# Kernel tuning notes

Measured on AMD Instinct MI355X. Metric: run time of the kernel, lower is better.

The kernel has to match this reference:

```python
import jax, jax.numpy as jnp
import numpy as np

EPS = 1e-12
B, CNT = 4096, 2048

def setup_inputs() -> dict:
    key = jax.random.key(0)
    k1, k2, k3 = jax.random.split(key, 3)
    timestampns_set = jax.random.uniform(k1, (B, CNT), dtype=jnp.float32)
    gyro_set = jax.random.normal(k2, (B, CNT, 3), dtype=jnp.float32)
    start_quat = jax.random.normal(k3, (B, 4), dtype=jnp.float32)
    # conv1/conv2 reduce to 3x3 linear maps on the xyz axis; initialized to identity, bias 0
    W1 = jnp.eye(3, dtype=jnp.float32)
    b1 = jnp.zeros((3,), dtype=jnp.float32)
    a1 = jnp.float32(0.25)  # PReLU default, single shared parameter
    W2 = jnp.eye(3, dtype=jnp.float32)
    b2 = jnp.zeros((3,), dtype=jnp.float32)
    a2 = jnp.float32(0.25)
    return {"timestampns_set": timestampns_set, "gyro_set": gyro_set,
            "start_quat": start_quat, "W1": W1, "b1": b1, "a1": a1,
            "W2": W2, "b2": b2, "a2": a2}

def _prelu(x, a):
    return jnp.where(x >= 0, x, a * x)

def _qmul(a, b):
    aw, ax, ay, az = a[:, 0], a[:, 1], a[:, 2], a[:, 3]
    bw, bx, by, bz = b[:, 0], b[:, 1], b[:, 2], b[:, 3]
    ow = aw * bw - ax * bx - ay * by - az * bz
    ox = aw * bx + ax * bw + ay * bz - az * by
    oy = aw * by - ax * bz + ay * bw + az * bx
    oz = aw * bz + ax * by - ay * bx + az * bw
    return jnp.stack((ow, ox, oy, oz), axis=-1)

def reference(timestampns_set, gyro_set, start_quat, W1, b1, a1, W2, b2, a2):
    # calibrate_gyro: two identity-init 3x3 'convs' + PReLU, residual add
    h = _prelu(jnp.einsum('btc,oc->bto', gyro_set, W1) + b1, a1)
    g = _prelu(jnp.einsum('btc,oc->bto', h, W2) + b2, a2) + gyro_set  # [B,CNT,3]
    dt = timestampns_set[:, 1:] - timestampns_set[:, :-1]             # [B,CNT-1]
    gm = 0.5 * (g[:, :-1, :] + g[:, 1:, :])                            # midpoint gyro
    dtheta_half = gm * dt[:, :, None] * 0.5                           # [B,CNT-1,3]

    def step(q, d):
        dq = jnp.concatenate([jnp.ones((d.shape[0], 1), d.dtype), d], axis=1)
        q = _qmul(q, dq)
        n = jnp.sqrt(jnp.sum(q * q, axis=1, keepdims=True))
        q = q / jnp.maximum(n, EPS)  # F.normalize semantics
        return q, None

    q, _ = jax.lax.scan(step, start_quat, jnp.swapaxes(dtheta_half, 0, 1))
    return q
```

## Files before the change

### kernel.cpp

```cpp
#include <hip/hip_runtime.h>

#define CNT   2048
#define NSTEP 2047
#define TPB   256
#define CHUNK 8
#define NWAVE (TPB / 64)

struct Q { float w, x, y, z; };

__device__ inline Q qmul(const Q a, const Q b) {
    Q o;
    o.w = a.w*b.w - a.x*b.x - a.y*b.y - a.z*b.z;
    o.x = a.w*b.x + a.x*b.w + a.y*b.z - a.z*b.y;
    o.y = a.w*b.y - a.x*b.z + a.y*b.w + a.z*b.x;
    o.z = a.w*b.z + a.x*b.y - a.y*b.x + a.z*b.w;
    return o;
}

__device__ inline Q qmul1(const Q a, const float bx, const float by, const float bz) {
    Q o;
    o.w = a.w - (a.x*bx + a.y*by + a.z*bz);
    o.x = a.x + (a.w*bx + a.y*bz - a.z*by);
    o.y = a.y + (a.w*by - a.x*bz + a.z*bx);
    o.z = a.z + (a.w*bz + a.x*by - a.y*bx);
    return o;
}

__global__ __launch_bounds__(TPB) void quat_scan_kernel(
    const float* __restrict__ ts,
    const float* __restrict__ gyro,
    const float* __restrict__ sq,
    const float* __restrict__ W1, const float* __restrict__ b1, const float* __restrict__ a1p,
    const float* __restrict__ W2, const float* __restrict__ b2, const float* __restrict__ a2p,
    float* __restrict__ out)
{
    __shared__ Q s_q[NWAVE];

    const int b    = blockIdx.x;
    const int tid  = threadIdx.x;
    const int t0   = tid * CHUNK;
    const bool last = (tid == TPB - 1);

    float rg[28];
    {
        const float4* gp = (const float4*)(gyro + (size_t)b * (CNT * 3) + (size_t)t0 * 3);
        #pragma unroll
        for (int k = 0; k < 6; ++k) ((float4*)rg)[k] = gp[k];
        if (!last) {
            ((float4*)rg)[6] = gp[6];
        } else {
            ((float4*)rg)[6] = make_float4(0.f, 0.f, 0.f, 0.f);
        }
    }
    float rt[9];
    {
        const float4* tp = (const float4*)(ts + (size_t)b * CNT + t0);
        #pragma unroll
        for (int k = 0; k < 2; ++k) ((float4*)&rt[0])[k] = tp[k];
        rt[8] = last ? rt[7] : ts[(size_t)b * CNT + t0 + 8];
    }

    float w1[9], w2[9], bb1[3], bb2[3];
    #pragma unroll
    for (int i = 0; i < 9; ++i) { w1[i] = W1[i]; w2[i] = W2[i]; }
    #pragma unroll
    for (int i = 0; i < 3; ++i) { bb1[i] = b1[i]; bb2[i] = b2[i]; }
    const float a1 = a1p[0], a2 = a2p[0];

    auto gf = [&](int j, float& gx, float& gy, float& gz) {
        const float vx = rg[3*j + 0], vy = rg[3*j + 1], vz = rg[3*j + 2];
        float h0 = w1[0]*vx + w1[1]*vy + w1[2]*vz + bb1[0];
        float h1 = w1[3]*vx + w1[4]*vy + w1[5]*vz + bb1[1];
        float h2 = w1[6]*vx + w1[7]*vy + w1[8]*vz + bb1[2];
        h0 = h0 >= 0.0f ? h0 : a1 * h0;
        h1 = h1 >= 0.0f ? h1 : a1 * h1;
        h2 = h2 >= 0.0f ? h2 : a1 * h2;
        float u0 = w2[0]*h0 + w2[1]*h1 + w2[2]*h2 + bb2[0];
        float u1 = w2[3]*h0 + w2[4]*h1 + w2[5]*h2 + bb2[1];
        float u2 = w2[6]*h0 + w2[7]*h1 + w2[8]*h2 + bb2[2];
        u0 = u0 >= 0.0f ? u0 : a2 * u0;
        u1 = u1 >= 0.0f ? u1 : a2 * u1;
        u2 = u2 >= 0.0f ? u2 : a2 * u2;
        gx = u0 + vx; gy = u1 + vy; gz = u2 + vz;
    };

    Q q = {1.0f, 0.0f, 0.0f, 0.0f};
    float g0x, g0y, g0z;
    gf(0, g0x, g0y, g0z);
    #pragma unroll
    for (int j = 0; j < CHUNK; ++j) {
        float g1x, g1y, g1z;
        gf(j + 1, g1x, g1y, g1z);
        const float s = 0.25f * (rt[j + 1] - rt[j]);
        q = qmul1(q, (g0x + g1x) * s, (g0y + g1y) * s, (g0z + g1z) * s);
        g0x = g1x; g0y = g1y; g0z = g1z;
    }

    {
        const float n2  = q.w*q.w + q.x*q.x + q.y*q.y + q.z*q.z;
        const float inv = 1.0f / sqrtf(n2);
        q.w *= inv; q.x *= inv; q.y *= inv; q.z *= inv;
    }

    #pragma unroll
    for (int sft = 1; sft < 64; sft <<= 1) {
        Q o;
        o.w = __shfl_down(q.w, sft);
        o.x = __shfl_down(q.x, sft);
        o.y = __shfl_down(q.y, sft);
        o.z = __shfl_down(q.z, sft);
        q = qmul(q, o);
    }

    const int lane = tid & 63;
    const int wid  = tid >> 6;
    if (lane == 0) s_q[wid] = q;
    __syncthreads();

    if (tid == 0) {
        Q acc = s_q[0];
        #pragma unroll
        for (int w = 1; w < NWAVE; ++w) acc = qmul(acc, s_q[w]);

        const float4 s0 = ((const float4*)(sq + (size_t)b * 4))[0];
        const Q q0 = {s0.x, s0.y, s0.z, s0.w};
        Q qf = qmul(q0, acc);
        const float n   = sqrtf(qf.w*qf.w + qf.x*qf.x + qf.y*qf.y + qf.z*qf.z);
        const float inv = 1.0f / fmaxf(n, 1e-12f);
        float4 o;
        o.x = qf.w * inv; o.y = qf.x * inv; o.z = qf.y * inv; o.w = qf.z * inv;
        ((float4*)(out + (size_t)b * 4))[0] = o;
    }
}

extern "C" void kernel_launch(void* const* d_in, const int* in_sizes, int n_in,
                              void* d_out, int out_size, void* d_ws, size_t ws_size,
                              hipStream_t stream) {
    const float* ts   = (const float*)d_in[0];
    const float* gyro = (const float*)d_in[1];
    const float* sq   = (const float*)d_in[2];
    const float* W1   = (const float*)d_in[3];
    const float* b1   = (const float*)d_in[4];
    const float* a1   = (const float*)d_in[5];
    const float* W2   = (const float*)d_in[6];
    const float* b2   = (const float*)d_in[7];
    const float* a2   = (const float*)d_in[8];
    float* out = (float*)d_out;

    const int B = in_sizes[0] / CNT;

    quat_scan_kernel<<<B, TPB, 0, stream>>>(ts, gyro, sq, W1, b1, a1, W2, b2, a2, out);
}
```

Measured before the change: 185.9 us.

## Use one wave per row with double-buffered async global-to-LDS segment loads

Each batch row is now handled by a single 64-lane wave instead of a 256-thread block. The row is processed in 8 segments of 256 steps, streamed into LDS with global_load_lds and double-buffered so the next segment's loads overlap the current segment's compute. Each segment is reduced with a wave-level quaternion shuffle scan, and the segment products are accumulated in order. This removes the __syncthreads and shared-memory cross-wave combine, but it adds 8 shuffle reductions per row and relies on manually encoded waitcnt values.

```diff
diff --git a/kernel.cpp b/kernel.cpp
--- a/kernel.cpp
+++ b/kernel.cpp
@@ -1,14 +1,13 @@
 #include <hip/hip_runtime.h>
 
 #define CNT   2048
-#define NSTEP 2047
-#define TPB   256
-#define CHUNK 8
-#define NWAVE (TPB / 64)
+#define TPB   64
+#define NSEG  8
+#define SMEM_F 2560
 
 struct Q { float w, x, y, z; };
 
-__device__ inline Q qmul(const Q a, const Q b) {
+__device__ __forceinline__ Q qmul(const Q a, const Q b) {
     Q o;
     o.w = a.w*b.w - a.x*b.x - a.y*b.y - a.z*b.z;
     o.x = a.w*b.x + a.x*b.w + a.y*b.z - a.z*b.y;
@@ -16,14 +15,36 @@
     o.z = a.w*b.z + a.x*b.y - a.y*b.x + a.z*b.w;
     return o;
 }
-
-__device__ inline Q qmul1(const Q a, const float bx, const float by, const float bz) {
+__device__ __forceinline__ Q qmul1(const Q a, const float bx, const float by, const float bz) {
     Q o;
     o.w = a.w - (a.x*bx + a.y*by + a.z*bz);
     o.x = a.x + (a.w*bx + a.y*bz - a.z*by);
     o.y = a.y + (a.w*by - a.x*bz + a.z*bx);
     o.z = a.z + (a.w*bz + a.x*by - a.y*bx);
     return o;
+}
+
+typedef __attribute__((address_space(1))) const void GAS;
+typedef __attribute__((address_space(3))) void LAS;
+
+__device__ __forceinline__ void cp16(const void* g, void* l) {
+    __builtin_amdgcn_global_load_lds((GAS*)g, (LAS*)l, 16, 0, 0);
+}
+__device__ __forceinline__ void wait_vm5() { __builtin_amdgcn_s_waitcnt(0x0F75); }
+__device__ __forceinline__ void wait_vm4() { __builtin_amdgcn_s_waitcnt(0x0F74); }
+__device__ __forceinline__ void wait_vm0() { __builtin_amdgcn_s_waitcnt(0x0F70); }
+
+__device__ __forceinline__ void issue_seg(const char* grow, const char* trow,
+                                          float* smem, int s, int lane) {
+    char* gslot = (char*)(smem + ((s & 1) ? 1024 : 0));
+    char* tslot = (char*)(smem + 2048 + ((s & 1) ? 256 : 0));
+    const char* gs = grow + 3072 * s + 16 * lane;
+    const char* tsr = trow + 1024 * s + 16 * lane;
+    cp16(gs,        gslot);
+    cp16(gs + 1024, gslot + 1024);
+    cp16(gs + 2048, gslot + 2048);
+    if (s != 7) cp16(gs + 3072, gslot + 3072);
+    cp16(tsr, tslot);
 }
 
 __global__ __launch_bounds__(TPB) void quat_scan_kernel(
@@ -34,31 +55,13 @@
     const float* __restrict__ W2, const float* __restrict__ b2, const float* __restrict__ a2p,
     float* __restrict__ out)
 {
-    __shared__ Q s_q[NWAVE];
+    __shared__ float smem[SMEM_F];
 
     const int b    = blockIdx.x;
-    const int tid  = threadIdx.x;
-    const int t0   = tid * CHUNK;
-    const bool last = (tid == TPB - 1);
+    const int lane = threadIdx.x;
 
-    float rg[28];
-    {
-        const float4* gp = (const float4*)(gyro + (size_t)b * (CNT * 3) + (size_t)t0 * 3);
-        #pragma unroll
-        for (int k = 0; k < 6; ++k) ((float4*)rg)[k] = gp[k];
-        if (!last) {
-            ((float4*)rg)[6] = gp[6];
-        } else {
-            ((float4*)rg)[6] = make_float4(0.f, 0.f, 0.f, 0.f);
-        }
-    }
-    float rt[9];
-    {
-        const float4* tp = (const float4*)(ts + (size_t)b * CNT + t0);
-        #pragma unroll
-        for (int k = 0; k < 2; ++k) ((float4*)&rt[0])[k] = tp[k];
-        rt[8] = last ? rt[7] : ts[(size_t)b * CNT + t0 + 8];
-    }
+    const char* grow = (const char*)(gyro + (size_t)b * (CNT * 3));
+    const char* trow = (const char*)(ts   + (size_t)b * CNT);
 
     float w1[9], w2[9], bb1[3], bb2[3];
     #pragma unroll
@@ -67,8 +70,12 @@
     for (int i = 0; i < 3; ++i) { bb1[i] = b1[i]; bb2[i] = b2[i]; }
     const float a1 = a1p[0], a2 = a2p[0];
 
-    auto gf = [&](int j, float& gx, float& gy, float& gz) {
-        const float vx = rg[3*j + 0], vy = rg[3*j + 1], vz = rg[3*j + 2];
+    const float* trowf = (const float*)trow;
+    int bidx = 256 * (lane + 1); if (bidx > 2047) bidx = 2047;
+    const float tbound = trowf[bidx];
+
+    auto gf = [&](const float* rg, int k, float& gx, float& gy, float& gz) {
+        const float vx = rg[3*k + 0], vy = rg[3*k + 1], vz = rg[3*k + 2];
         float h0 = w1[0]*vx + w1[1]*vy + w1[2]*vz + bb1[0];
         float h1 = w1[3]*vx + w1[4]*vy + w1[5]*vz + bb1[1];
         float h2 = w1[6]*vx + w1[7]*vy + w1[8]*vz + bb1[2];
@@ -84,52 +91,76 @@
         gx = u0 + vx; gy = u1 + vy; gz = u2 + vz;
     };
 
-    Q q = {1.0f, 0.0f, 0.0f, 0.0f};
-    float g0x, g0y, g0z;
-    gf(0, g0x, g0y, g0z);
-    #pragma unroll
-    for (int j = 0; j < CHUNK; ++j) {
-        float g1x, g1y, g1z;
-        gf(j + 1, g1x, g1y, g1z);
-        const float s = 0.25f * (rt[j + 1] - rt[j]);
-        q = qmul1(q, (g0x + g1x) * s, (g0y + g1y) * s, (g0z + g1z) * s);
-        g0x = g1x; g0y = g1y; g0z = g1z;
+    Q qrow = {1.0f, 0.0f, 0.0f, 0.0f};
+
+    auto do_seg = [&](int s, bool fix_last) {
+        const float* gb = smem + ((s & 1) ? 1024 : 0);
+        const float* tb = smem + 2048 + ((s & 1) ? 256 : 0);
+
+        float rg[16];
+        const float4* gp4 = (const float4*)(gb + 12 * lane);
+        #pragma unroll
+        for (int k = 0; k < 4; ++k) ((float4*)rg)[k] = gp4[k];
+
+        float rt[5];
+        *((float4*)rt) = *((const float4*)(tb + 4 * lane));
+        float rt4 = tb[4 * lane + 4];
+        const float bnd = __shfl(tbound, s & 7);
+        rt[4] = (lane == 63) ? bnd : rt4;
+
+        if (fix_last && lane == 63) {
+            rg[12] = rg[9]; rg[13] = rg[10]; rg[14] = rg[11];
+            rt[4]  = rt[3];
+        }
+
+        Q P = {1.0f, 0.0f, 0.0f, 0.0f};
+        float g0x, g0y, g0z;
+        gf(rg, 0, g0x, g0y, g0z);
+        #pragma unroll
+        for (int j = 0; j < 4; ++j) {
+            float g1x, g1y, g1z;
+            gf(rg, j + 1, g1x, g1y, g1z);
+            const float sc = 0.25f * (rt[j + 1] - rt[j]);
+            P = qmul1(P, (g0x + g1x) * sc, (g0y + g1y) * sc, (g0z + g1z) * sc);
+            g0x = g1x; g0y = g1y; g0z = g1z;
+        }
+        const float n2  = P.w*P.w + P.x*P.x + P.y*P.y + P.z*P.z;
+        const float inv = 1.0f / sqrtf(n2);
+        P.w *= inv; P.x *= inv; P.y *= inv; P.z *= inv;
+
+        #pragma unroll
+        for (int sft = 1; sft < 64; sft <<= 1) {
+            Q o;
+            o.w = __shfl_down(P.w, sft);
+            o.x = __shfl_down(P.x, sft);
+            o.y = __shfl_down(P.y, sft);
+            o.z = __shfl_down(P.z, sft);
+            P = qmul(P, o);
+        }
+        qrow = qmul(qrow, P);
+    };
+
+    issue_seg(grow, trow, smem, 0, lane);
+    issue_seg(grow, trow, smem, 1, lane);
+    for (int s = 0; s < 6; ++s) {
+        wait_vm5();
+        do_seg(s, false);
+        issue_seg(grow, trow, smem, s + 2, lane);
     }
+    wait_vm4();
+    do_seg(6, false);
+    wait_vm0();
+    do_seg(7, true);
 
-    {
-        const float n2  = q.w*q.w + q.x*q.x + q.y*q.y + q.z*q.z;
-        const float inv = 1.0f / sqrtf(n2);
-        q.w *= inv; q.x *= inv; q.y *= inv; q.z *= inv;
-    }
-
-    #pragma unroll
-    for (int sft = 1; sft < 64; sft <<= 1) {
-        Q o;
-        o.w = __shfl_down(q.w, sft);
-        o.x = __shfl_down(q.x, sft);
-        o.y = __shfl_down(q.y, sft);
-        o.z = __shfl_down(q.z, sft);
-        q = qmul(q, o);
-    }
-
-    const int lane = tid & 63;
-    const int wid  = tid >> 6;
-    if (lane == 0) s_q[wid] = q;
-    __syncthreads();
-
-    if (tid == 0) {
-        Q acc = s_q[0];
-        #pragma unroll
-        for (int w = 1; w < NWAVE; ++w) acc = qmul(acc, s_q[w]);
-
-        const float4 s0 = ((const float4*)(sq + (size_t)b * 4))[0];
+    if (lane == 0) {
+        const float4 s0 = *((const float4*)(sq + (size_t)b * 4));
         const Q q0 = {s0.x, s0.y, s0.z, s0.w};
-        Q qf = qmul(q0, acc);
+        Q qf = qmul(q0, qrow);
         const float n   = sqrtf(qf.w*qf.w + qf.x*qf.x + qf.y*qf.y + qf.z*qf.z);
         const float inv = 1.0f / fmaxf(n, 1e-12f);
         float4 o;
         o.x = qf.w * inv; o.y = qf.x * inv; o.z = qf.y * inv; o.w = qf.z * inv;
-        ((float4*)(out + (size_t)b * 4))[0] = o;
+        *((float4*)(out + (size_t)b * 4)) = o;
     }
 }
 
```

After: 194.9 us. 1.05x slower.

## Split scan into persistent wave-per-segment pass plus combine pass, with identity fast path

Applied to the files above, without the earlier changes.

Restructures the kernel so each wavefront handles one quarter-row segment in a grid-stride persistent loop, with software prefetching of the next segment's inputs into registers. Per-segment quaternion products go to workspace, and a second small kernel multiplies the four segments and applies the start quaternion. This removes the block-level shared memory and barrier and is meant to improve latency hiding. It also adds a runtime check that skips the 3x3 matmuls when the weights are exactly identity with zero bias. The cost is an extra kernel launch and higher register pressure from the double buffers.

```diff
diff --git a/kernel.cpp b/kernel.cpp
--- a/kernel.cpp
+++ b/kernel.cpp
@@ -1,14 +1,14 @@
 #include <hip/hip_runtime.h>
 
-#define CNT   2048
-#define NSTEP 2047
-#define TPB   256
-#define CHUNK 8
-#define NWAVE (TPB / 64)
+#define CNT    2048
+#define NSTEP  2047
+#define TPB    256
+#define BLOCKS 2048
+#define WPB    (TPB / 64)
 
 struct Q { float w, x, y, z; };
 
-__device__ inline Q qmul(const Q a, const Q b) {
+__device__ __forceinline__ Q qmul(const Q a, const Q b) {
     Q o;
     o.w = a.w*b.w - a.x*b.x - a.y*b.y - a.z*b.z;
     o.x = a.w*b.x + a.x*b.w + a.y*b.z - a.z*b.y;
@@ -16,8 +16,7 @@
     o.z = a.w*b.z + a.x*b.y - a.y*b.x + a.z*b.w;
     return o;
 }
-
-__device__ inline Q qmul1(const Q a, const float bx, const float by, const float bz) {
+__device__ __forceinline__ Q qmul1(const Q a, const float bx, const float by, const float bz) {
     Q o;
     o.w = a.w - (a.x*bx + a.y*by + a.z*bz);
     o.x = a.x + (a.w*bx + a.y*bz - a.z*by);
@@ -26,39 +25,78 @@
     return o;
 }
 
-__global__ __launch_bounds__(TPB) void quat_scan_kernel(
+template<bool FAST>
+__device__ __forceinline__ void gf_eval(const float* rg, int k,
+        const float* w1, const float* bb1, float a1,
+        const float* w2, const float* bb2, float a2,
+        float& gx, float& gy, float& gz)
+{
+    const float vx = rg[3*k + 0], vy = rg[3*k + 1], vz = rg[3*k + 2];
+    float h0, h1, h2;
+    if (FAST) { h0 = vx; h1 = vy; h2 = vz; }
+    else {
+        h0 = w1[0]*vx + w1[1]*vy + w1[2]*vz + bb1[0];
+        h1 = w1[3]*vx + w1[4]*vy + w1[5]*vz + bb1[1];
+        h2 = w1[6]*vx + w1[7]*vy + w1[8]*vz + bb1[2];
+    }
+    h0 = h0 >= 0.0f ? h0 : a1 * h0;
+    h1 = h1 >= 0.0f ? h1 : a1 * h1;
+    h2 = h2 >= 0.0f ? h2 : a1 * h2;
+    float u0, u1, u2;
+    if (FAST) { u0 = h0; u1 = h1; u2 = h2; }
+    else {
+        u0 = w2[0]*h0 + w2[1]*h1 + w2[2]*h2 + bb2[0];
+        u1 = w2[3]*h0 + w2[4]*h1 + w2[5]*h2 + bb2[1];
+        u2 = w2[6]*h0 + w2[7]*h1 + w2[8]*h2 + bb2[2];
+    }
+    u0 = u0 >= 0.0f ? u0 : a2 * u0;
+    u1 = u1 >= 0.0f ? u1 : a2 * u1;
+    u2 = u2 >= 0.0f ? u2 : a2 * u2;
+    gx = u0 + vx; gy = u1 + vy; gz = u2 + vz;
+}
+
+template<bool FAST>
+__device__ __forceinline__ Q seg_product(const float* rg, const float* rt,
+        const float* w1, const float* bb1, float a1,
+        const float* w2, const float* bb2, float a2)
+{
+    Q P = {1.0f, 0.0f, 0.0f, 0.0f};
+    float g0x, g0y, g0z;
+    gf_eval<FAST>(rg, 0, w1, bb1, a1, w2, bb2, a2, g0x, g0y, g0z);
+    #pragma unroll
+    for (int j = 0; j < 8; ++j) {
+        float g1x, g1y, g1z;
+        gf_eval<FAST>(rg, j + 1, w1, bb1, a1, w2, bb2, a2, g1x, g1y, g1z);
+        const float sc = 0.25f * (rt[j + 1] - rt[j]);
+        P = qmul1(P, (g0x + g1x) * sc, (g0y + g1y) * sc, (g0z + g1z) * sc);
+        g0x = g1x; g0y = g1y; g0z = g1z;
+    }
+    const float n2  = P.w*P.w + P.x*P.x + P.y*P.y + P.z*P.z;
+    const float inv = 1.0f / sqrtf(n2);
+    P.w *= inv; P.x *= inv; P.y *= inv; P.z *= inv;
+    #pragma unroll
+    for (int sft = 1; sft < 64; sft <<= 1) {
+        Q o;
+        o.w = __shfl_down(P.w, sft);
+        o.x = __shfl_down(P.x, sft);
+        o.y = __shfl_down(P.y, sft);
+        o.z = __shfl_down(P.z, sft);
+        P = qmul(P, o);
+    }
+    return P;
+}
+
+__global__ __launch_bounds__(TPB) void pass1_kernel(
     const float* __restrict__ ts,
     const float* __restrict__ gyro,
-    const float* __restrict__ sq,
     const float* __restrict__ W1, const float* __restrict__ b1, const float* __restrict__ a1p,
     const float* __restrict__ W2, const float* __restrict__ b2, const float* __restrict__ a2p,
-    float* __restrict__ out)
+    float4* __restrict__ ws,
+    int nitems)
 {
-    __shared__ Q s_q[NWAVE];
-
-    const int b    = blockIdx.x;
-    const int tid  = threadIdx.x;
-    const int t0   = tid * CHUNK;
-    const bool last = (tid == TPB - 1);
-
-    float rg[28];
-    {
-        const float4* gp = (const float4*)(gyro + (size_t)b * (CNT * 3) + (size_t)t0 * 3);
-        #pragma unroll
-        for (int k = 0; k < 6; ++k) ((float4*)rg)[k] = gp[k];
-        if (!last) {
-            ((float4*)rg)[6] = gp[6];
-        } else {
-            ((float4*)rg)[6] = make_float4(0.f, 0.f, 0.f, 0.f);
-        }
-    }
-    float rt[9];
-    {
-        const float4* tp = (const float4*)(ts + (size_t)b * CNT + t0);
-        #pragma unroll
-        for (int k = 0; k < 2; ++k) ((float4*)&rt[0])[k] = tp[k];
-        rt[8] = last ? rt[7] : ts[(size_t)b * CNT + t0 + 8];
-    }
+    const int lane = threadIdx.x & 63;
+    const int wgid = blockIdx.x * WPB + (threadIdx.x >> 6);
+    const int nw   = gridDim.x * WPB;
 
     float w1[9], w2[9], bb1[3], bb2[3];
     #pragma unroll
@@ -67,70 +105,72 @@
     for (int i = 0; i < 3; ++i) { bb1[i] = b1[i]; bb2[i] = b2[i]; }
     const float a1 = a1p[0], a2 = a2p[0];
 
-    auto gf = [&](int j, float& gx, float& gy, float& gz) {
-        const float vx = rg[3*j + 0], vy = rg[3*j + 1], vz = rg[3*j + 2];
-        float h0 = w1[0]*vx + w1[1]*vy + w1[2]*vz + bb1[0];
-        float h1 = w1[3]*vx + w1[4]*vy + w1[5]*vz + bb1[1];
-        float h2 = w1[6]*vx + w1[7]*vy + w1[8]*vz + bb1[2];
-        h0 = h0 >= 0.0f ? h0 : a1 * h0;
-        h1 = h1 >= 0.0f ? h1 : a1 * h1;
-        h2 = h2 >= 0.0f ? h2 : a1 * h2;
-        float u0 = w2[0]*h0 + w2[1]*h1 + w2[2]*h2 + bb2[0];
-        float u1 = w2[3]*h0 + w2[4]*h1 + w2[5]*h2 + bb2[1];
-        float u2 = w2[6]*h0 + w2[7]*h1 + w2[8]*h2 + bb2[2];
-        u0 = u0 >= 0.0f ? u0 : a2 * u0;
-        u1 = u1 >= 0.0f ? u1 : a2 * u1;
-        u2 = u2 >= 0.0f ? u2 : a2 * u2;
-        gx = u0 + vx; gy = u1 + vy; gz = u2 + vz;
+    float dev = 0.0f;
+    #pragma unroll
+    for (int i = 0; i < 9; ++i) {
+        const float id = (i == 0 || i == 4 || i == 8) ? 1.0f : 0.0f;
+        dev += fabsf(w1[i] - id) + fabsf(w2[i] - id);
+    }
+    #pragma unroll
+    for (int i = 0; i < 3; ++i) dev += fabsf(bb1[i]) + fabsf(bb2[i]);
+    const bool fast = (dev == 0.0f);
+
+    auto loadit = [&](int item, float* rg, float* rt) {
+        const int r = item >> 2, s = item & 3;
+        const bool last = (s == 3) && (lane == 63);
+        const float4* gp = (const float4*)(gyro + (size_t)r * (CNT * 3)) + (384 * s + 6 * lane);
+        #pragma unroll
+        for (int k = 0; k < 6; ++k) ((float4*)rg)[k] = gp[k];
+        ((float4*)rg)[6] = last ? make_float4(0.f, 0.f, 0.f, 0.f) : gp[6];
+        const float* trow = ts + (size_t)r * CNT + (512 * s + 8 * lane);
+        ((float4*)rt)[0] = ((const float4*)trow)[0];
+        ((float4*)rt)[1] = ((const float4*)trow)[1];
+        rt[8] = last ? rt[7] : trow[8];
     };
 
-    Q q = {1.0f, 0.0f, 0.0f, 0.0f};
-    float g0x, g0y, g0z;
-    gf(0, g0x, g0y, g0z);
+    float rgA[28], rtA[9];
+    int item = wgid;
+    if (item < nitems) loadit(item, rgA, rtA);
+
+    for (; item < nitems; item += nw) {
+        const int nxt = item + nw;
+        float rgB[28], rtB[9];
+        if (nxt < nitems) loadit(nxt, rgB, rtB);
+
+        Q P = fast ? seg_product<true >(rgA, rtA, w1, bb1, a1, w2, bb2, a2)
+                   : seg_product<false>(rgA, rtA, w1, bb1, a1, w2, bb2, a2);
+        if (lane == 0) ws[item] = make_float4(P.w, P.x, P.y, P.z);
+
+        #pragma unroll
+        for (int i = 0; i < 28; ++i) rgA[i] = rgB[i];
+        #pragma unroll
+        for (int i = 0; i < 9; ++i)  rtA[i] = rtB[i];
+    }
+}
+
+__global__ __launch_bounds__(TPB) void pass2_kernel(
+    const float4* __restrict__ ws,
+    const float*  __restrict__ sq,
+    float* __restrict__ out, int B)
+{
+    const int r = blockIdx.x * blockDim.x + threadIdx.x;
+    if (r >= B) return;
+    float4 p0 = ws[4*r + 0];
+    Q acc = {p0.x, p0.y, p0.z, p0.w};
     #pragma unroll
-    for (int j = 0; j < CHUNK; ++j) {
-        float g1x, g1y, g1z;
-        gf(j + 1, g1x, g1y, g1z);
-        const float s = 0.25f * (rt[j + 1] - rt[j]);
-        q = qmul1(q, (g0x + g1x) * s, (g0y + g1y) * s, (g0z + g1z) * s);
-        g0x = g1x; g0y = g1y; g0z = g1z;
+    for (int k = 1; k < 4; ++k) {
+        const float4 pk = ws[4*r + k];
+        const Q qk = {pk.x, pk.y, pk.z, pk.w};
+        acc = qmul(acc, qk);
     }
-
-    {
-        const float n2  = q.w*q.w + q.x*q.x + q.y*q.y + q.z*q.z;
-        const float inv = 1.0f / sqrtf(n2);
-        q.w *= inv; q.x *= inv; q.y *= inv; q.z *= inv;
-    }
-
-    #pragma unroll
-    for (int sft = 1; sft < 64; sft <<= 1) {
-        Q o;
-        o.w = __shfl_down(q.w, sft);
-        o.x = __shfl_down(q.x, sft);
-        o.y = __shfl_down(q.y, sft);
-        o.z = __shfl_down(q.z, sft);
-        q = qmul(q, o);
-    }
-
-    const int lane = tid & 63;
-    const int wid  = tid >> 6;
-    if (lane == 0) s_q[wid] = q;
-    __syncthreads();
-
-    if (tid == 0) {
-        Q acc = s_q[0];
-        #pragma unroll
-        for (int w = 1; w < NWAVE; ++w) acc = qmul(acc, s_q[w]);
-
-        const float4 s0 = ((const float4*)(sq + (size_t)b * 4))[0];
-        const Q q0 = {s0.x, s0.y, s0.z, s0.w};
-        Q qf = qmul(q0, acc);
-        const float n   = sqrtf(qf.w*qf.w + qf.x*qf.x + qf.y*qf.y + qf.z*qf.z);
-        const float inv = 1.0f / fmaxf(n, 1e-12f);
-        float4 o;
-        o.x = qf.w * inv; o.y = qf.x * inv; o.z = qf.y * inv; o.w = qf.z * inv;
-        ((float4*)(out + (size_t)b * 4))[0] = o;
-    }
+    const float4 s0 = ((const float4*)sq)[r];
+    const Q q0 = {s0.x, s0.y, s0.z, s0.w};
+    Q qf = qmul(q0, acc);
+    const float n   = sqrtf(qf.w*qf.w + qf.x*qf.x + qf.y*qf.y + qf.z*qf.z);
+    const float inv = 1.0f / fmaxf(n, 1e-12f);
+    float4 o;
+    o.x = qf.w * inv; o.y = qf.x * inv; o.z = qf.y * inv; o.w = qf.z * inv;
+    ((float4*)out)[r] = o;
 }
 
 extern "C" void kernel_launch(void* const* d_in, const int* in_sizes, int n_in,
@@ -147,7 +187,10 @@
     const float* a2   = (const float*)d_in[8];
     float* out = (float*)d_out;
 
-    const int B = in_sizes[0] / CNT;
+    const int B      = in_sizes[0] / CNT;
+    const int nitems = B * 4;
+    float4* ws = (float4*)d_ws;
 
-    quat_scan_kernel<<<B, TPB, 0, stream>>>(ts, gyro, sq, W1, b1, a1, W2, b2, a2, out);
+    pass1_kernel<<<BLOCKS, TPB, 0, stream>>>(ts, gyro, W1, b1, a1, W2, b2, a2, ws, nitems);
+    pass2_kernel<<<(B + TPB - 1) / TPB, TPB, 0, stream>>>(ws, sq, out, B);
 }
```

After: 192.5 us. +3.5%, slower.
